# Kernel tuning notes

Hardware: AMD Instinct MI355X
Metric: run time of the kernel (lower is better)

The kernel has to match this reference:

```python
import jax, jax.numpy as jnp
import numpy as np

B, T, D, H = 128, 256, 256, 1024
DEC_STEPS = 59


def _gates(g):
    # torch LSTM gate order: input, forget, cell(g), output
    i, f, gg, o = jnp.split(g, 4, axis=-1)
    return jax.nn.sigmoid(i), jax.nn.sigmoid(f), jnp.tanh(gg), jax.nn.sigmoid(o)


def _cell(x, h, c, W_ih, W_hh, b_ih, b_hh):
    g = x @ W_ih.T + b_ih + h @ W_hh.T + b_hh
    i, f, gg, o = _gates(g)
    c = f * c + i * gg
    h = o * jnp.tanh(c)
    return h, c


def _layer(x, W_ih, W_hh, b_ih, b_hh):
    # x: [B, T, Din] -> outputs [B, T, H], final (h, c)
    b, hdim = x.shape[0], W_hh.shape[1]
    xp = jnp.einsum('btd,gd->btg', x, W_ih) + b_ih  # precompute input proj [B,T,4H]

    def step(carry, xt):
        h, c = carry
        g = xt + h @ W_hh.T + b_hh
        i, f, gg, o = _gates(g)
        c = f * c + i * gg
        h = o * jnp.tanh(c)
        return (h, c), h

    h0 = jnp.zeros((b, hdim), x.dtype)
    (hT, cT), hs = jax.lax.scan(step, (h0, h0), jnp.swapaxes(xp, 0, 1))
    return jnp.swapaxes(hs, 0, 1), hT, cT


def setup_inputs() -> dict:
    key = jax.random.key(0)
    ks = jax.random.split(key, 12)
    s = 1.0 / np.sqrt(H)
    u = lambda k, shape: jax.random.uniform(k, shape, jnp.float32, -s, s)
    return {
        'x': jax.random.normal(ks[0], (B, T, D), jnp.float32),
        'W_ih0': u(ks[1], (4 * H, D)),
        'W_hh0': u(ks[2], (4 * H, H)),
        'b_ih0': u(ks[3], (4 * H,)),
        'b_hh0': u(ks[4], (4 * H,)),
        'W_ih1': u(ks[5], (4 * H, H)),
        'W_hh1': u(ks[6], (4 * H, H)),
        'b_ih1': u(ks[7], (4 * H,)),
        'b_hh1': u(ks[8], (4 * H,)),
        'W_lin': u(ks[9], (D, H)),
        'b_lin': u(ks[10], (D,)),
    }


def reference(x, W_ih0, W_hh0, b_ih0, b_hh0, W_ih1, W_hh1, b_ih1, b_hh1, W_lin, b_lin):
    out0, h0, c0 = _layer(x, W_ih0, W_hh0, b_ih0, b_hh0)
    out1, h1, c1 = _layer(out0, W_ih1, W_hh1, b_ih1, b_hh1)
    y_last = out1[:, -1, :] @ W_lin.T + b_lin  # [B, D]

    def dec(carry, _):
        h0_, c0_, h1_, c1_, y = carry
        h0_, c0_ = _cell(y, h0_, c0_, W_ih0, W_hh0, b_ih0, b_hh0)
        h1_, c1_ = _cell(h0_, h1_, c1_, W_ih1, W_hh1, b_ih1, b_hh1)
        y = h1_ @ W_lin.T + b_lin
        return (h0_, c0_, h1_, c1_, y), y

    _, ys = jax.lax.scan(dec, (h0, c0, h1, c1, y_last), None, length=DEC_STEPS)
    ys = jnp.swapaxes(ys, 0, 1)  # [B, 59, D]
    # original returns y[:, T-1:, :] => last prefix prediction + 59 decoded steps
    return jnp.concatenate([y_last[:, None, :], ys], axis=1)  # [B, 60, D]
```

## Files before the change

### kernel.cpp

```cpp
#include <hip/hip_runtime.h>
#include <hip/hip_bf16.h>
#include <cstdint>


typedef _Float16 half_t;
typedef _Float16 half8 __attribute__((ext_vector_type(8)));
typedef float float4v __attribute__((ext_vector_type(4)));
typedef int int32x4_t __attribute__((ext_vector_type(4)));
typedef float float32x4_t __attribute__((ext_vector_type(4)));

__device__ float32x4_t llvm_amdgcn_raw_buffer_load_fp32x4(
    int32x4_t srsrc, int voffset, int soffset, int aux)
    __asm("llvm.amdgcn.raw.buffer.load.v4f32");

#define AUX_SC1 16

union SrdU { int32x4_t v; struct { const void* p; unsigned nr, fl; } s; };
__device__ __forceinline__ int32x4_t make_srd(const void* p) {
  SrdU u; u.s.p = p; u.s.nr = 0xFFFFFFFFu; u.s.fl = 0x00020000u; return u.v;
}

__device__ __forceinline__ unsigned poll4(const int* p) {
  union { float32x4_t f; int i[4]; } u;
  u.f = llvm_amdgcn_raw_buffer_load_fp32x4(make_srd(p), 0, 0, AUX_SC1);
  unsigned m = 0;
  if (u.i[0] >= 16) m |= 1u;
  if (u.i[1] >= 16) m |= 2u;
  if (u.i[2] >= 16) m |= 4u;
  if (u.i[3] >= 16) m |= 8u;
  return m;
}

__device__ __forceinline__ unsigned peek8(const int* f) {
  return poll4(f) | (poll4(f + 4) << 4);
}

__device__ __forceinline__ void wait_chunk(const int* f, int c, unsigned& got) {
  if (!((got >> c) & 1)) {
    for (;;) {
      got |= peek8(f);
      if ((got >> c) & 1) break;
      __builtin_amdgcn_s_sleep(2);
    }
  }
  asm volatile("" ::: "memory");
}

__device__ __forceinline__ void flag_add(int* p) {
  __hip_atomic_fetch_add(p, 1, __ATOMIC_RELAXED, __HIP_MEMORY_SCOPE_AGENT);
}

__device__ __forceinline__ float sigm_(float x) { return 1.0f / (1.0f + __expf(-x)); }
__device__ __forceinline__ float tanh_(float x) {
  float ax = fabsf(x);
  float e = __expf(-2.0f * ax);
  float t = (1.0f - e) / (1.0f + e);
  return x < 0.0f ? -t : t;
}

#define MFMA16(a, b, c) __builtin_amdgcn_mfma_f32_16x16x32_f16(a, b, c, 0, 0, 0)


__device__ __forceinline__ void issue_chunk(const half_t* __restrict__ A, int c,
                                            int ro, half8 (&a0)[4], half8 (&a1)[4]) {
#pragma unroll
  for (int k4 = 0; k4 < 4; ++k4) {
    const half_t* ap = A + (c * 16 + k4 * 4) * 1024 + ro;
    a0[k4] = *(const half8*)ap;
    a1[k4] = *(const half8*)(ap + 128);
  }
}

__device__ __forceinline__ void consume_chunk(const half8 (&a0)[4],
                                              const half8 (&a1)[4],
                                              const half_t* __restrict__ W, int kk0,
                                              int lq, int lrow, float4v acc[2][2]) {
#pragma unroll
  for (int k4 = 0; k4 < 4; ++k4) {
    const half_t* bp = W + (kk0 + k4) * 1024 + lq * 256 + lrow * 8;
    half8 b0 = *(const half8*)bp;
    half8 b1 = *(const half8*)(bp + 128);
    acc[0][0] = MFMA16(a0[k4], b0, acc[0][0]);
    acc[0][1] = MFMA16(a0[k4], b1, acc[0][1]);
    acc[1][0] = MFMA16(a1[k4], b0, acc[1][0]);
    acc[1][1] = MFMA16(a1[k4], b1, acc[1][1]);
  }
}

template <int NC>
__device__ __forceinline__ void issue_chunks(const half_t* __restrict__ A, int ro,
                                             half8 (&a0)[NC][4], half8 (&a1)[NC][4]) {
#pragma unroll
  for (int c = 0; c < NC; ++c) issue_chunk(A, c, ro, a0[c], a1[c]);
}

template <int NC>
__device__ __forceinline__ void consume_chunks(const half8 (&a0)[NC][4],
                                               const half8 (&a1)[NC][4],
                                               const half_t* __restrict__ W, int kk0,
                                               int lq, int lrow, float4v acc[2][2]) {
#pragma unroll
  for (int c = 0; c < NC; ++c)
    consume_chunk(a0[c], a1[c], W, kk0 + c * 4, lq, lrow, acc);
}

__device__ __forceinline__ void stream8g(const half_t* __restrict__ A,
                                         const half_t* __restrict__ W, int kk0,
                                         const int* f, unsigned got,
                                         int ro, int lq, int lrow, float4v acc[2][2]) {
  half8 a0[4][4], a1[4][4];
#pragma unroll
  for (int c = 0; c < 4; ++c) {
    wait_chunk(f, c, got);
    issue_chunk(A, c, ro, a0[c], a1[c]);
  }
#pragma unroll
  for (int c = 0; c < 8; ++c) {
    consume_chunk(a0[c & 3], a1[c & 3], W, kk0 + c * 4, lq, lrow, acc);
    if (c < 4) {
      wait_chunk(f, c + 4, got);
      issue_chunk(A, c + 4, ro, a0[c & 3], a1[c & 3]);
    }
  }
}

__device__ __forceinline__ void stream_l0p(const half_t* __restrict__ XHs,
                                           const half_t* __restrict__ A,
                                           const half_t* __restrict__ W,
                                           const int* f, int ro, int lq, int lrow,
                                           float4v acc[2][2]) {
  half8 xa0[2][4], xa1[2][4];
  issue_chunks<2>(XHs, ro, xa0, xa1);
  unsigned got = peek8(f);
  half8 a0[4][4], a1[4][4];
#pragma unroll
  for (int c = 0; c < 4; ++c) {
    wait_chunk(f, c, got);
    issue_chunk(A, c, ro, a0[c], a1[c]);
  }
  consume_chunk(xa0[0], xa1[0], W, 0, lq, lrow, acc);
  consume_chunk(xa0[1], xa1[1], W, 4, lq, lrow, acc);
#pragma unroll
  for (int c = 0; c < 8; ++c) {
    consume_chunk(a0[c & 3], a1[c & 3], W, 8 + c * 4, lq, lrow, acc);
    if (c < 4) {
      wait_chunk(f, c + 4, got);
      issue_chunk(A, c + 4, ro, a0[c & 3], a1[c & 3]);
    }
  }
}

__device__ __forceinline__ void epi_gates(
    float4v acc[2][2], int tile, const float* __restrict__ biasArr,
    float c[2][2], half_t* hTile, half_t* __restrict__ hDst, int tid) {
  const int l = tid & 63, rg = tid >> 6;
  const int lrow = l & 15, lq = l >> 4, q = l & 3, a = lrow >> 2;
  __syncthreads();
#pragma unroll
  for (int m = 0; m < 2; ++m)
#pragma unroll
    for (int nf = 0; nf < 2; ++nf) {
      const float bias = biasArr[tile * 32 + nf * 16 + lrow];
      float gi = 0.f, gf = 0.f, gg = 0.f, go = 0.f;
#pragma unroll
      for (int r = 0; r < 4; ++r) {
        float x = acc[m][nf][r] + bias;
        float t1 = __shfl_xor(x, 1);
        float t2 = __shfl_xor(x, 2);
        float t3 = __shfl_xor(x, 3);
        if (r == q) {
          gi = (q == 0) ? x : (q == 1 ? t1 : (q == 2 ? t2 : t3));
          gf = (q == 1) ? x : (q == 0 ? t1 : (q == 3 ? t2 : t3));
          gg = (q == 2) ? x : (q == 3 ? t1 : (q == 0 ? t2 : t3));
          go = (q == 3) ? x : (q == 2 ? t1 : (q == 1 ? t2 : t3));
        }
      }
      const int row = rg * 32 + m * 16 + lq * 4 + q;
      const int ju = nf * 4 + a;
      float iv = sigm_(gi), fv = sigm_(gf), gv = tanh_(gg), ov = sigm_(go);
      float cnew = fv * c[m][nf] + iv * gv;
      c[m][nf] = cnew;
      hTile[row * 8 + ju] = (half_t)(ov * tanh_(cnew));
    }
  __syncthreads();
  if (tid < 128) {
    const unsigned long long* s = (const unsigned long long*)(hTile + tid * 8);
    unsigned long long v0 = s[0], v1 = s[1];
    unsigned long long* d = (unsigned long long*)(hDst + tid * 8);
    __hip_atomic_store(d, v0, __ATOMIC_RELAXED, __HIP_MEMORY_SCOPE_AGENT);
    __hip_atomic_store(d + 1, v1, __ATOMIC_RELAXED, __HIP_MEMORY_SCOPE_AGENT);
  }
}

__device__ __forceinline__ void epi_y(
    float4v acc[2][2], int ytile, int i, const float* __restrict__ biasY,
    float* __restrict__ out, int tid) {
  const int l = tid & 63, rg = tid >> 6;
  const int lrow = l & 15, lq = l >> 4;
#pragma unroll
  for (int m = 0; m < 2; ++m)
#pragma unroll
    for (int nf = 0; nf < 2; ++nf) {
      const int d = ytile * 32 + nf * 16 + lrow;
      const float b = biasY[d];
#pragma unroll
      for (int r = 0; r < 4; ++r) {
        const int row = rg * 32 + m * 16 + lq * 4 + r;
        out[(long)row * 15360 + i * 256 + d] = acc[m][nf][r] + b;
      }
    }
}

__device__ __forceinline__ void loadW(const half_t* __restrict__ src,
                                      half_t* dst, int halves, int tid) {
  for (int i = tid * 8; i < halves; i += 2048)
    *(uint4*)(dst + i) = *(const uint4*)(src + i);
}

#define ZACC2 float4v acc[2][2]; { float4v z = {0.f, 0.f, 0.f, 0.f}; \
  acc[0][0] = z; acc[0][1] = z; acc[1][0] = z; acc[1][1] = z; }

__global__ void __launch_bounds__(256, 1) k_lstm(
    const half_t* __restrict__ S0, const half_t* __restrict__ S1,
    const half_t* __restrict__ SD, const half_t* __restrict__ SY,
    const half_t* __restrict__ XH,
    half_t* __restrict__ H0, half_t* __restrict__ H1,
    const float* __restrict__ B0P, const float* __restrict__ B1P,
    const float* __restrict__ BD0P, float* __restrict__ out, int* FLGB) {
  __shared__ char smem[133120];
  half_t* ldsW = (half_t*)smem;
  half_t* hTile = (half_t*)(smem + 131072);
  const int w = blockIdx.x, tid = threadIdx.x;
  const int l = tid & 63, rg = tid >> 6;
  const int lrow = l & 15, lq = l >> 4;
  const int ro = (rg * 32 + lrow) * 8 + lq * 1024;
  float c2[2][2] = {{0.f, 0.f}, {0.f, 0.f}};
#define SLOTP(base, idx) ((base) + (long)(idx) * 131072)
#define FREC(s, lay, rr) (FLGB + ((((s) * 2 + (lay)) * 4 + (rr)) << 5))

  if (w < 128) {
    const int g = w >> 4;
    loadW(S0 + (long)w * 40960, ldsW, 40960, tid);
    __syncthreads();
    {
      ZACC2;
      half8 xa0[2][4], xa1[2][4];
      issue_chunks<2>(XH, ro, xa0, xa1);
      consume_chunks<2>(xa0, xa1, ldsW, 0, lq, lrow, acc);
      epi_gates(acc, w, B0P, c2, hTile, SLOTP(H0, 1) + w * 1024, tid);
      __syncthreads();
      if ((tid & 63) == 0) flag_add(FREC(0, 0, rg) + g);
    }
    for (int s = 1; s < 256; ++s) {
      ZACC2;
      stream_l0p(XH + (long)s * 32768, SLOTP(H0, s), ldsW, FREC(s - 1, 0, rg),
                 ro, lq, lrow, acc);
      epi_gates(acc, w, B0P, c2, hTile, SLOTP(H0, s + 1) + w * 1024, tid);
      __syncthreads();
      if ((tid & 63) == 0) flag_add(FREC(s, 0, rg) + g);
    }
    __syncthreads();
    loadW(SD + (long)w * 65536, ldsW, 65536, tid);
    __syncthreads();
    for (int i = 0; i < 59; ++i) {
      ZACC2;
      const int* fF = FREC(256 + i, 1, rg);
      const int* fO = FREC(255 + i, 0, rg);
      unsigned gotO = peek8(fO);
      stream8g(SLOTP(H1, 256 + i), ldsW, 0, fF, 0u, ro, lq, lrow, acc);
      stream8g(SLOTP(H0, 256 + i), ldsW, 32, fO, gotO, ro, lq, lrow, acc);
      epi_gates(acc, w, BD0P, c2, hTile, SLOTP(H0, 257 + i) + w * 1024, tid);
      __syncthreads();
      if ((tid & 63) == 0) flag_add(FREC(256 + i, 0, rg) + g);
    }
  } else {
    const int bw = w - 128, g = bw >> 4;
    loadW(S1 + (long)bw * 65536, ldsW, 65536, tid);
    __syncthreads();
    for (int s = 1; s <= 256; ++s) {
      ZACC2;
      const int* fF = FREC(s - 1, 0, rg);
      const int* fO = FREC(s - 1, 1, rg);
      unsigned gotO = (s >= 2) ? peek8(fO) : 0u;
      stream8g(SLOTP(H0, s), ldsW, 0, fF, 0u, ro, lq, lrow, acc);
      if (s >= 2)
        stream8g(SLOTP(H1, s - 1), ldsW, 32, fO, gotO, ro, lq, lrow, acc);
      epi_gates(acc, bw, B1P, c2, hTile, SLOTP(H1, s) + bw * 1024, tid);
      __syncthreads();
      if ((tid & 63) == 0) flag_add(FREC(s, 1, rg) + g);
    }
    for (int i = 0; i < 59; ++i) {
      ZACC2;
      const int* fF = FREC(256 + i, 0, rg);
      const int* fO = FREC(256 + i, 1, rg);
      unsigned gotO = peek8(fO);
      stream8g(SLOTP(H0, 257 + i), ldsW, 0, fF, 0u, ro, lq, lrow, acc);
      stream8g(SLOTP(H1, 256 + i), ldsW, 32, fO, gotO, ro, lq, lrow, acc);
      epi_gates(acc, bw, B1P, c2, hTile, SLOTP(H1, 257 + i) + bw * 1024, tid);
      __syncthreads();
      if ((tid & 63) == 0) flag_add(FREC(257 + i, 1, rg) + g);
    }
  }

  for (int j = w; j < 480; j += 256) {
    const int i = j >> 3, t = j & 7;
    ZACC2;
    const int* f = FREC(256 + i, 1, rg);
    stream8g(SLOTP(H1, 256 + i), SY + (long)t * 32768, 0, f, peek8(f),
             ro, lq, lrow, acc);
    epi_y(acc, t, i, BD0P + 4096, out, tid);
  }
#undef FREC
#undef SLOTP
}


__global__ void k_cvt_x(const float* __restrict__ x, half_t* __restrict__ XH) {
  int idx = blockIdx.x * 256 + threadIdx.x;
  int t = idx >> 12;
  int kb = (idx >> 7) & 31;
  int r = idx & 127;
  const float* src = x + ((long)((r << 8) + t)) * 256 + kb * 8;
  float4 v0 = *(const float4*)src;
  float4 v1 = *(const float4*)(src + 4);
  half_t tmp[8] = {(half_t)v0.x, (half_t)v0.y, (half_t)v0.z, (half_t)v0.w,
                   (half_t)v1.x, (half_t)v1.y, (half_t)v1.z, (half_t)v1.w};
  *(uint4*)(XH + (long)t * 32768 + kb * 1024 + r * 8) = *(const uint4*)tmp;
}

__global__ void k_pack32(const float* __restrict__ A, int KA,
                         const float* __restrict__ Bsrc,
                         half_t* __restrict__ dst, int KT32, int skipA) {
  int idx = blockIdx.x * 256 + threadIdx.x;
  int nn = idx & 31;
  int lq = (idx >> 5) & 3;
  int t2 = idx >> 7;
  int kk = t2 % KT32;
  int tile = t2 / KT32;
  if (tile >= 128) return;
  int k = kk * 32 + lq * 8;
  int rp = tile * 32 + nn;
  int r = ((rp & 3) << 10) + (rp >> 2);
  const float* src;
  if (k < KA) {
    if (skipA) return;
    src = A + (long)r * KA + k;
  } else {
    src = Bsrc + (long)r * 1024 + (k - KA);
  }
  float4 v0 = *(const float4*)src;
  float4 v1 = *(const float4*)(src + 4);
  half_t tmp[8] = {(half_t)v0.x, (half_t)v0.y, (half_t)v0.z, (half_t)v0.w,
                   (half_t)v1.x, (half_t)v1.y, (half_t)v1.z, (half_t)v1.w};
  *(uint4*)(dst + (long)tile * (KT32 * 1024) + kk * 1024 + lq * 256 + nn * 8) =
      *(const uint4*)tmp;
}

__global__ void k_pack_y32(const float* __restrict__ Wlin,
                           half_t* __restrict__ SY) {
  int idx = blockIdx.x * 256 + threadIdx.x;
  int nn = idx & 31;
  int lq = (idx >> 5) & 3;
  int kk = (idx >> 7) & 31;
  int tile = idx >> 12;
  int d = tile * 32 + nn;
  int k = kk * 32 + lq * 8;
  const float* src = Wlin + (long)d * 1024 + k;
  float4 v0 = *(const float4*)src;
  float4 v1 = *(const float4*)(src + 4);
  half_t tmp[8] = {(half_t)v0.x, (half_t)v0.y, (half_t)v0.z, (half_t)v0.w,
                   (half_t)v1.x, (half_t)v1.y, (half_t)v1.z, (half_t)v1.w};
  *(uint4*)(SY + (long)tile * 32768 + kk * 1024 + lq * 256 + nn * 8) =
      *(const uint4*)tmp;
}

__global__ void k_bias_simple(const float* bi0, const float* bh0,
                              const float* bi1, const float* bh1,
                              const float* blin, float* b0p, float* b1p,
                              float* bD0p) {
  int rp = blockIdx.x * blockDim.x + threadIdx.x;
  if (rp < 4096) {
    int r = ((rp & 3) << 10) + (rp >> 2);
    b0p[rp] = bi0[r] + bh0[r];
    b1p[rp] = bi1[r] + bh1[r];
  } else if (rp < 4352) {
    bD0p[rp] = blin[rp - 4096];
  }
}

__global__ void k_bias_dot(const float* __restrict__ Wih0,
                           const float* __restrict__ blin,
                           const float* __restrict__ bi0,
                           const float* __restrict__ bh0,
                           float* __restrict__ bD0p) {
  int wv = threadIdx.x >> 6, l = threadIdx.x & 63;
  int r = blockIdx.x * 4 + wv;
  float s = 0.f;
#pragma unroll
  for (int c = 0; c < 4; ++c) s += Wih0[r * 256 + c * 64 + l] * blin[c * 64 + l];
#pragma unroll
  for (int o = 32; o >= 1; o >>= 1) s += __shfl_xor(s, o);
  if (l == 0) {
    int rp = ((r & 1023) << 2) | (r >> 10);
    bD0p[rp] = bi0[r] + bh0[r] + s;
  }
}

__global__ void k_weff(const float* __restrict__ Wih0,
                       const float* __restrict__ Wlin,
                       half_t* __restrict__ SD) {
  __shared__ float At[64][65];
  __shared__ float Bt[64][65];
  const int rt = blockIdx.x, jt = blockIdx.y;
  const int tid = threadIdx.x;
  const int tx = tid & 15, ty = tid >> 4;
  float acc[4][4] = {};
  for (int k0 = 0; k0 < 256; k0 += 64) {
    __syncthreads();
#pragma unroll
    for (int i = 0; i < 16; ++i) {
      int lin = tid + 256 * i;
      int rr = lin >> 6, kk = lin & 63;
      At[rr][kk] = Wih0[(rt * 64 + rr) * 256 + k0 + kk];
      Bt[rr][kk] = Wlin[(k0 + rr) * 1024 + jt * 64 + kk];
    }
    __syncthreads();
    for (int kk = 0; kk < 64; ++kk) {
      float a[4], b[4];
#pragma unroll
      for (int i = 0; i < 4; ++i) a[i] = At[ty * 4 + i][kk];
#pragma unroll
      for (int i = 0; i < 4; ++i) b[i] = Bt[kk][tx * 4 + i];
#pragma unroll
      for (int i = 0; i < 4; ++i)
#pragma unroll
        for (int jx = 0; jx < 4; ++jx) acc[i][jx] += a[i] * b[jx];
    }
  }
#pragma unroll
  for (int i = 0; i < 4; ++i) {
    int r = rt * 64 + ty * 4 + i;
    int rp = ((r & 1023) << 2) | (r >> 10);
    int tile = rp >> 5, nn = rp & 31;
#pragma unroll
    for (int jx = 0; jx < 4; ++jx) {
      int j = jt * 64 + tx * 4 + jx;
      SD[(long)tile * 65536 + (j >> 5) * 1024 + ((j >> 3) & 3) * 256 + nn * 8 +
         (j & 7)] = (half_t)acc[i][jx];
    }
  }
}


extern "C" void kernel_launch(void* const* d_in, const int* in_sizes, int n_in,
                              void* d_out, int out_size, void* d_ws, size_t ws_size,
                              hipStream_t stream) {
  (void)in_sizes; (void)n_in; (void)out_size; (void)ws_size;
  const float* x    = (const float*)d_in[0];
  const float* Wih0 = (const float*)d_in[1];
  const float* Whh0 = (const float*)d_in[2];
  const float* bi0  = (const float*)d_in[3];
  const float* bh0  = (const float*)d_in[4];
  const float* Wih1 = (const float*)d_in[5];
  const float* Whh1 = (const float*)d_in[6];
  const float* bi1  = (const float*)d_in[7];
  const float* bh1  = (const float*)d_in[8];
  const float* Wlin = (const float*)d_in[9];
  const float* blin = (const float*)d_in[10];
  float* out = (float*)d_out;
  char* ws = (char*)d_ws;

  half_t* S0  = (half_t*)(ws + 0);
  half_t* S1  = (half_t*)(ws + 10485760);
  half_t* SD  = (half_t*)(ws + 27262976);
  half_t* SY  = (half_t*)(ws + 44040192);
  half_t* XH  = (half_t*)(ws + 44564480);
  float*  B0P = (float*)(ws + 61341696);
  float*  B1P = (float*)(ws + 61358080);
  float*  BD0P= (float*)(ws + 61374464);
  half_t* H0  = (half_t*)(ws + 61432320);
  half_t* H1  = (half_t*)(ws + 145318400);
  int*    FLGB= (int*)(ws + 145318400 + (long)316 * 262144);

  hipMemsetAsync(FLGB, 0, 327680, stream);
  hipMemsetAsync(H0, 0, 262144, stream);
  hipMemsetAsync(H1, 0, 262144, stream);

  k_cvt_x<<<4096, 256, 0, stream>>>(x, XH);
  k_bias_simple<<<17, 256, 0, stream>>>(bi0, bh0, bi1, bh1, blin, B0P, B1P, BD0P);
  k_bias_dot<<<1024, 256, 0, stream>>>(Wih0, blin, bi0, bh0, BD0P);
  k_pack32<<<2560, 256, 0, stream>>>(Wih0, 256, Whh0, S0, 40, 0);
  k_pack32<<<4096, 256, 0, stream>>>(Wih1, 1024, Whh1, S1, 64, 0);
  k_pack32<<<4096, 256, 0, stream>>>(nullptr, 1024, Whh0, SD, 64, 1);
  k_pack_y32<<<128, 256, 0, stream>>>(Wlin, SY);
  k_weff<<<dim3(64, 16), 256, 0, stream>>>(Wih0, Wlin, SD);

  k_lstm<<<256, 256, 0, stream>>>(S0, S1, SD, SY, XH, H0, H1,
                                  B0P, B1P, BD0P, out, FLGB);
}
```

Before: 4.667 ms.

## Replace block-wide barriers in gate epilogue with per-wavefront LDS tiles and stores

Each wavefront now writes its own 32-row slice of the h tile into a private LDS region and stores it to global memory itself. This replaces the two __syncthreads per step with explicit s_waitcnt instructions. Each wavefront can then signal its row-group flag on its own, without waiting for the whole block. The goal is to cut barrier stalls on the serial recurrence critical path. It relies on the wavefront-local LDS ordering holding and on the per-row-group flags matching the per-wave data ownership.

```diff
diff --git a/kernel.cpp b/kernel.cpp
--- a/kernel.cpp
+++ b/kernel.cpp
@@ -152,10 +152,8 @@
 
 __device__ __forceinline__ void epi_gates(
     float4v acc[2][2], int tile, const float* __restrict__ biasArr,
-    float c[2][2], half_t* hTile, half_t* __restrict__ hDst, int tid) {
-  const int l = tid & 63, rg = tid >> 6;
+    float c[2][2], half_t* hTileW, half_t* __restrict__ hDstW, int l) {
   const int lrow = l & 15, lq = l >> 4, q = l & 3, a = lrow >> 2;
-  __syncthreads();
 #pragma unroll
   for (int m = 0; m < 2; ++m)
 #pragma unroll
@@ -175,21 +173,21 @@
           go = (q == 3) ? x : (q == 2 ? t1 : (q == 1 ? t2 : t3));
         }
       }
-      const int row = rg * 32 + m * 16 + lq * 4 + q;
+      const int lr = m * 16 + lq * 4 + q;
       const int ju = nf * 4 + a;
       float iv = sigm_(gi), fv = sigm_(gf), gv = tanh_(gg), ov = sigm_(go);
       float cnew = fv * c[m][nf] + iv * gv;
       c[m][nf] = cnew;
-      hTile[row * 8 + ju] = (half_t)(ov * tanh_(cnew));
-    }
-  __syncthreads();
-  if (tid < 128) {
-    const unsigned long long* s = (const unsigned long long*)(hTile + tid * 8);
-    unsigned long long v0 = s[0], v1 = s[1];
-    unsigned long long* d = (unsigned long long*)(hDst + tid * 8);
-    __hip_atomic_store(d, v0, __ATOMIC_RELAXED, __HIP_MEMORY_SCOPE_AGENT);
-    __hip_atomic_store(d + 1, v1, __ATOMIC_RELAXED, __HIP_MEMORY_SCOPE_AGENT);
-  }
+      hTileW[lr * 8 + ju] = (half_t)(ov * tanh_(cnew));
+    }
+  asm volatile("s_waitcnt lgkmcnt(0)" ::: "memory");
+  {
+    const int r = l >> 1, hh = l & 1;
+    unsigned long long v = *(const unsigned long long*)(hTileW + r * 8 + hh * 4);
+    unsigned long long* d = (unsigned long long*)(hDstW + r * 8 + hh * 4);
+    __hip_atomic_store(d, v, __ATOMIC_RELAXED, __HIP_MEMORY_SCOPE_AGENT);
+  }
+  asm volatile("s_waitcnt vmcnt(0)" ::: "memory");
 }
 
 __device__ __forceinline__ void epi_y(
@@ -229,11 +227,12 @@
     const float* __restrict__ BD0P, float* __restrict__ out, int* FLGB) {
   __shared__ char smem[133120];
   half_t* ldsW = (half_t*)smem;
-  half_t* hTile = (half_t*)(smem + 131072);
   const int w = blockIdx.x, tid = threadIdx.x;
   const int l = tid & 63, rg = tid >> 6;
   const int lrow = l & 15, lq = l >> 4;
   const int ro = (rg * 32 + lrow) * 8 + lq * 1024;
+  half_t* hTileW = (half_t*)(smem + 131072) + rg * 256;
+  const int hOffW = rg * 256;
   float c2[2][2] = {{0.f, 0.f}, {0.f, 0.f}};
 #define SLOTP(base, idx) ((base) + (long)(idx) * 131072)
 #define FREC(s, lay, rr) (FLGB + ((((s) * 2 + (lay)) * 4 + (rr)) << 5))
@@ -247,17 +246,15 @@
       half8 xa0[2][4], xa1[2][4];
       issue_chunks<2>(XH, ro, xa0, xa1);
       consume_chunks<2>(xa0, xa1, ldsW, 0, lq, lrow, acc);
-      epi_gates(acc, w, B0P, c2, hTile, SLOTP(H0, 1) + w * 1024, tid);
-      __syncthreads();
-      if ((tid & 63) == 0) flag_add(FREC(0, 0, rg) + g);
+      epi_gates(acc, w, B0P, c2, hTileW, SLOTP(H0, 1) + w * 1024 + hOffW, l);
+      if (l == 0) flag_add(FREC(0, 0, rg) + g);
     }
     for (int s = 1; s < 256; ++s) {
       ZACC2;
       stream_l0p(XH + (long)s * 32768, SLOTP(H0, s), ldsW, FREC(s - 1, 0, rg),
                  ro, lq, lrow, acc);
-      epi_gates(acc, w, B0P, c2, hTile, SLOTP(H0, s + 1) + w * 1024, tid);
-      __syncthreads();
-      if ((tid & 63) == 0) flag_add(FREC(s, 0, rg) + g);
+      epi_gates(acc, w, B0P, c2, hTileW, SLOTP(H0, s + 1) + w * 1024 + hOffW, l);
+      if (l == 0) flag_add(FREC(s, 0, rg) + g);
     }
     __syncthreads();
     loadW(SD + (long)w * 65536, ldsW, 65536, tid);
@@ -269,9 +266,9 @@
       unsigned gotO = peek8(fO);
       stream8g(SLOTP(H1, 256 + i), ldsW, 0, fF, 0u, ro, lq, lrow, acc);
       stream8g(SLOTP(H0, 256 + i), ldsW, 32, fO, gotO, ro, lq, lrow, acc);
-      epi_gates(acc, w, BD0P, c2, hTile, SLOTP(H0, 257 + i) + w * 1024, tid);
-      __syncthreads();
-      if ((tid & 63) == 0) flag_add(FREC(256 + i, 0, rg) + g);
+      epi_gates(acc, w, BD0P, c2, hTileW,
+                SLOTP(H0, 257 + i) + w * 1024 + hOffW, l);
+      if (l == 0) flag_add(FREC(256 + i, 0, rg) + g);
     }
   } else {
     const int bw = w - 128, g = bw >> 4;
@@ -285,9 +282,9 @@
       stream8g(SLOTP(H0, s), ldsW, 0, fF, 0u, ro, lq, lrow, acc);
       if (s >= 2)
         stream8g(SLOTP(H1, s - 1), ldsW, 32, fO, gotO, ro, lq, lrow, acc);
-      epi_gates(acc, bw, B1P, c2, hTile, SLOTP(H1, s) + bw * 1024, tid);
-      __syncthreads();
-      if ((tid & 63) == 0) flag_add(FREC(s, 1, rg) + g);
+      epi_gates(acc, bw, B1P, c2, hTileW,
+                SLOTP(H1, s) + bw * 1024 + hOffW, l);
+      if (l == 0) flag_add(FREC(s, 1, rg) + g);
     }
     for (int i = 0; i < 59; ++i) {
       ZACC2;
@@ -296,9 +293,9 @@
       unsigned gotO = peek8(fO);
       stream8g(SLOTP(H0, 257 + i), ldsW, 0, fF, 0u, ro, lq, lrow, acc);
       stream8g(SLOTP(H1, 256 + i), ldsW, 32, fO, gotO, ro, lq, lrow, acc);
-      epi_gates(acc, bw, B1P, c2, hTile, SLOTP(H1, 257 + i) + bw * 1024, tid);
-      __syncthreads();
-      if ((tid & 63) == 0) flag_add(FREC(257 + i, 1, rg) + g);
+      epi_gates(acc, bw, B1P, c2, hTileW,
+                SLOTP(H1, 257 + i) + bw * 1024 + hOffW, l);
+      if (l == 0) flag_add(FREC(257 + i, 1, rg) + g);
     }
   }
 
```

New measurement: 9.880 ms. 2.12x slower.
